# Kernel optimization log

Measured on AMD Instinct MI355X. Metric: run time of the kernel, lower is better.

## Reference

```python
import jax, jax.numpy as jnp
import numpy as np

DIM = 512
HEADS = 16
WIN = (2, 7, 7)
N = WIN[0] * WIN[1] * WIN[2]  # 98
TABLE = (2 * WIN[0] - 1) * (2 * WIN[1] - 1) * (2 * WIN[2] - 1)  # 507


def _rel_pos_index():
    cd, ch, cw = np.arange(WIN[0]), np.arange(WIN[1]), np.arange(WIN[2])
    coords = np.stack(np.meshgrid(cd, ch, cw, indexing='ij'))  # (3, D, H, W)
    flat = coords.reshape(3, -1)  # (3, N)
    rel = flat[:, :, None] - flat[:, None, :]  # (3, N, N)
    rel = rel.transpose(1, 2, 0).copy()
    rel[:, :, 0] += WIN[0] - 1
    rel[:, :, 1] += WIN[1] - 1
    rel[:, :, 2] += WIN[2] - 1
    rel[:, :, 0] *= (2 * WIN[1] - 1) * (2 * WIN[2] - 1)
    rel[:, :, 1] *= 2 * WIN[2] - 1
    return jnp.asarray(rel.sum(-1), dtype=jnp.int32)  # (N, N)


def setup_inputs() -> dict:
    key = jax.random.key(0)
    ks = jax.random.split(key, 7)
    B_ = 1024
    nW = 64
    return {
        'x': jax.random.normal(ks[0], (B_, N, DIM), dtype=jnp.float32),
        'mask': jnp.zeros((nW, N, N), dtype=jnp.float32),
        'qkv_w': jax.random.normal(ks[1], (3 * DIM, DIM), dtype=jnp.float32) * 0.02,
        'qkv_b': jnp.zeros((3 * DIM,), dtype=jnp.float32),
        'proj_w': jax.random.normal(ks[2], (DIM, DIM), dtype=jnp.float32) * 0.02,
        'proj_b': jnp.zeros((DIM,), dtype=jnp.float32),
        'bias_table': jax.random.normal(ks[3], (TABLE, HEADS), dtype=jnp.float32) * 0.02,
        'rel_pos_index': _rel_pos_index(),
    }


def reference(x, mask, qkv_w, qkv_b, proj_w, proj_b, bias_table, rel_pos_index):
    B_, n, C = x.shape
    hd = C // HEADS
    scale = hd ** -0.5
    # qkv projection: (B_, N, 3C) -> (3, B_, H, N, hd)
    qkv = (x @ qkv_w.T + qkv_b).reshape(B_, n, 3, HEADS, hd).transpose(2, 0, 3, 1, 4)
    q, k, v = qkv[0], qkv[1], qkv[2]
    attn = jnp.einsum('bhnd,bhmd->bhnm', q * scale, k)  # (B_, H, N, N)
    # gathered relative position bias: (N, N, H) -> (H, N, N)
    bias = bias_table[rel_pos_index.reshape(-1)].reshape(n, n, HEADS).transpose(2, 0, 1)
    attn = attn + bias[None]
    nW = mask.shape[0]
    attn = attn.reshape(B_ // nW, nW, HEADS, n, n) + mask[None, :, None]
    attn = jax.nn.softmax(attn.reshape(B_, HEADS, n, n), axis=-1)
    out = jnp.einsum('bhnm,bhmd->bnhd', attn, v).reshape(B_, n, C)
    return out @ proj_w.T + proj_b
```

## Files before the change

kernel.cpp:

```cpp
#include <hip/hip_runtime.h>
#include <hip/hip_bf16.h>
#include <stdint.h>

#define DIMC 512
#define NTOK 98

typedef float f32x4 __attribute__((ext_vector_type(4)));
typedef short bf16x8 __attribute__((ext_vector_type(8)));
typedef short bf16x4 __attribute__((ext_vector_type(4)));

__device__ inline unsigned short f2bf(float f) {
    union { float f; uint32_t u; } v; v.f = f;
    uint32_t r = v.u + 0x7fffu + ((v.u >> 16) & 1u);
    return (unsigned short)(r >> 16);
}

__device__ inline bf16x8 cvt8(float4 a, float4 b) {
    bf16x8 r;
    r[0] = (short)f2bf(a.x); r[1] = (short)f2bf(a.y);
    r[2] = (short)f2bf(a.z); r[3] = (short)f2bf(a.w);
    r[4] = (short)f2bf(b.x); r[5] = (short)f2bf(b.y);
    r[6] = (short)f2bf(b.z); r[7] = (short)f2bf(b.w);
    return r;
}

__device__ __forceinline__ void gload16(const void* g, void* l) {
    __builtin_amdgcn_global_load_lds(
        (const __attribute__((address_space(1))) unsigned int*)g,
        (__attribute__((address_space(3))) unsigned int*)l, 16, 0, 0);
}

#define CFENCE() __asm__ __volatile__("" ::: "memory")
#define BARRIER() do { CFENCE(); __builtin_amdgcn_s_barrier(); CFENCE(); } while (0)

__global__ void k_cvt3(const float* __restrict__ s0, unsigned short* __restrict__ d0,
                       const float* __restrict__ s1, unsigned short* __restrict__ d1,
                       const float* __restrict__ s2, unsigned short* __restrict__ d2) {
    int b = blockIdx.x;
    const float* src; unsigned short* dst; int i;
    if (b < 25088)      { src = s0; dst = d0; i = b * 256 + threadIdx.x; }
    else if (b < 25472) { src = s1; dst = d1; i = (b - 25088) * 256 + threadIdx.x; }
    else                { src = s2; dst = d2; i = (b - 25472) * 256 + threadIdx.x; }
    float4 a = *(const float4*)(src + (size_t)i * 8);
    float4 c = *(const float4*)(src + (size_t)i * 8 + 4);
    *(bf16x8*)(dst + (size_t)i * 8) = cvt8(a, c);
}

__global__ void k_bm2(const float* __restrict__ table, const int* __restrict__ idx,
                      const float* __restrict__ mask, float* __restrict__ bm_t) {
    int slice = blockIdx.x;
    int b64 = slice >> 4, h = slice & 15;
    float* dst = bm_t + (size_t)slice * 12544;
    const float* mp = mask + (size_t)b64 * 9604;
    for (int t = threadIdx.x; t < 12544; t += blockDim.x) {
        int i = t / 112, c = t - i * 112;
        float v = -1e9f;
        if (c < NTOK && i < NTOK)
            v = (table[idx[i * NTOK + c] * 16 + h] + mp[i * NTOK + c])
                * 1.4426950408889634f;
        dst[t] = v;
    }
}

__global__ __launch_bounds__(512, 2)
void k_qkv3(const unsigned short* __restrict__ xb, const unsigned short* __restrict__ wb,
            const float* __restrict__ qb, unsigned short* __restrict__ qkvbuf) {
    __shared__ unsigned short As[2][2][128 * 64];
    __shared__ unsigned short Bs[2][2][128 * 64];
    const int tid = threadIdx.x;
    const int wid = tid >> 6, l = tid & 63, g = l >> 4, li = l & 15;
    const int wm = wid >> 2, wn = wid & 3;
    const int id = blockIdx.x;
    const int xcd = id & 7, local = id >> 3;
    const int mt = xcd * 49 + local / 6;
    const int nt = local - (local / 6) * 6;
    const int m0 = mt * 256, n0 = nt * 256;

    const int srow = tid >> 3;
    const int scg  = tid & 7;
    const int sxor = (scg ^ (srow & 7)) * 8;
    const unsigned short* aG[2][2];
    const unsigned short* bG[2][2];
    #pragma unroll
    for (int h = 0; h < 2; ++h) {
        aG[h][0] = xb + (size_t)(m0 + h * 128 + srow) * DIMC + sxor;
        aG[h][1] = xb + (size_t)(m0 + h * 128 + 64 + srow) * DIMC + sxor;
        bG[h][0] = wb + (size_t)(n0 + h * 128 + srow) * DIMC + sxor;
        bG[h][1] = wb + (size_t)(n0 + h * 128 + 64 + srow) * DIMC + sxor;
    }
    const int lb0 = wid * 512;
    const int lb1 = 4096 + wid * 512;

    const int axor0 = ((0 + g) ^ (li & 7)) * 8;
    const int axor1 = ((4 + g) ^ (li & 7)) * 8;
    const int arow = li * 64;
    const int brow = (wn & 1) * 4096 + li * 64;
    const int bh = wn >> 1;

    f32x4 acc[8][4] = {};

    gload16(bG[0][0], &Bs[0][0][lb0]); gload16(bG[1][0], &Bs[0][1][lb0]);
    gload16(bG[0][1], &Bs[0][0][lb1]); gload16(bG[1][1], &Bs[0][1][lb1]);
    gload16(aG[0][0], &As[0][0][lb0]); gload16(aG[1][0], &As[0][1][lb0]);
    gload16(aG[0][1], &As[0][0][lb1]); gload16(aG[1][1], &As[0][1][lb1]);

    #pragma unroll
    for (int kt = 0; kt < 8; ++kt) {
        const int s = kt & 1, p = s ^ 1;
        const int ko = (kt + 1) * 64;
        bf16x8 bfr[4][2];
        #pragma unroll
        for (int q = 0; q < 4; ++q) {
            const int mq0 = 2 * q;
            bf16x8 a00, a01, a10, a11;
            if (q == 1 || q == 3) {
                a00 = *(const bf16x8*)&As[s][wm][arow + mq0 * 1024 + axor0];
                a01 = *(const bf16x8*)&As[s][wm][arow + mq0 * 1024 + axor1];
                a10 = *(const bf16x8*)&As[s][wm][arow + (mq0 + 1) * 1024 + axor0];
                a11 = *(const bf16x8*)&As[s][wm][arow + (mq0 + 1) * 1024 + axor1];
            }
            if (kt < 7) {
                if (q == 0) { gload16(bG[0][0] + ko, &Bs[p][0][lb0]);
                              gload16(bG[1][0] + ko, &Bs[p][1][lb0]); }
                if (q == 1) { gload16(bG[0][1] + ko, &Bs[p][0][lb1]);
                              gload16(bG[1][1] + ko, &Bs[p][1][lb1]); }
                if (q == 2) { gload16(aG[0][0] + ko, &As[p][0][lb0]);
                              gload16(aG[1][0] + ko, &As[p][1][lb0]); }
                if (q == 3) { gload16(aG[0][1] + ko, &As[p][0][lb1]);
                              gload16(aG[1][1] + ko, &As[p][1][lb1]); }
            }
            if (q == 0) {
                if (kt < 7) __asm__ __volatile__("s_waitcnt vmcnt(4)" ::: "memory");
                else        __asm__ __volatile__("s_waitcnt vmcnt(2)" ::: "memory");
            } else if (q == 2) {
                if (kt < 7) __asm__ __volatile__("s_waitcnt vmcnt(6)" ::: "memory");
                else        __asm__ __volatile__("s_waitcnt vmcnt(0)" ::: "memory");
            } else {
                if (kt < 7) __asm__ __volatile__("s_waitcnt vmcnt(6)" ::: "memory");
            }
            BARRIER();
            if (q == 0) {
                #pragma unroll
                for (int nq = 0; nq < 4; ++nq) {
                    bfr[nq][0] = *(const bf16x8*)&Bs[s][bh][brow + nq * 1024 + axor0];
                    bfr[nq][1] = *(const bf16x8*)&Bs[s][bh][brow + nq * 1024 + axor1];
                }
            }
            if (q == 0 || q == 2) {
                a00 = *(const bf16x8*)&As[s][wm][arow + mq0 * 1024 + axor0];
                a01 = *(const bf16x8*)&As[s][wm][arow + mq0 * 1024 + axor1];
                a10 = *(const bf16x8*)&As[s][wm][arow + (mq0 + 1) * 1024 + axor0];
                a11 = *(const bf16x8*)&As[s][wm][arow + (mq0 + 1) * 1024 + axor1];
            }
            __asm__ __volatile__("s_waitcnt lgkmcnt(0)" ::: "memory");
            __builtin_amdgcn_s_setprio(1);
            #pragma unroll
            for (int nq = 0; nq < 4; ++nq) {
                acc[mq0][nq] = __builtin_amdgcn_mfma_f32_16x16x32_bf16(
                    bfr[nq][0], a00, acc[mq0][nq], 0, 0, 0);
                acc[mq0][nq] = __builtin_amdgcn_mfma_f32_16x16x32_bf16(
                    bfr[nq][1], a01, acc[mq0][nq], 0, 0, 0);
                acc[mq0 + 1][nq] = __builtin_amdgcn_mfma_f32_16x16x32_bf16(
                    bfr[nq][0], a10, acc[mq0 + 1][nq], 0, 0, 0);
                acc[mq0 + 1][nq] = __builtin_amdgcn_mfma_f32_16x16x32_bf16(
                    bfr[nq][1], a11, acc[mq0 + 1][nq], 0, 0, 0);
            }
            __builtin_amdgcn_s_setprio(0);
        }
    }

    #pragma unroll
    for (int mq = 0; mq < 8; ++mq) {
        int row = m0 + wm * 128 + mq * 16 + li;
        unsigned bw = (unsigned)row / 98u;
        unsigned nn_ = (unsigned)row - bw * 98u;
        unsigned short* rbase = qkvbuf + (size_t)bw * 150528u + nn_ * 32u;
        #pragma unroll
        for (int nq = 0; nq < 4; ++nq) {
            int col0 = n0 + wn * 64 + nq * 16 + g * 4;
            int which = col0 >> 9;
            int h = (col0 >> 5) & 15;
            int d0 = col0 & 31;
            float4 bv = *(const float4*)(qb + col0);
            float sc = (which == 0)
                ? (0.17677669529663689f * 1.4426950408889634f) : 1.0f;
            bf16x4 pk;
            pk[0] = (short)f2bf((acc[mq][nq][0] + bv.x) * sc);
            pk[1] = (short)f2bf((acc[mq][nq][1] + bv.y) * sc);
            pk[2] = (short)f2bf((acc[mq][nq][2] + bv.z) * sc);
            pk[3] = (short)f2bf((acc[mq][nq][3] + bv.w) * sc);
            *(bf16x4*)(rbase + (size_t)(h * 3 + which) * 3136u + d0) = pk;
        }
    }
}

__global__ __launch_bounds__(512, 2)
void k_proj3(const unsigned short* __restrict__ qkvbuf,
             const unsigned short* __restrict__ wb,
             const float* __restrict__ pb, float* __restrict__ out) {
    __shared__ unsigned short As[2][2][128 * 64];
    __shared__ unsigned short Bs[2][2][128 * 64];
    const int tid = threadIdx.x;
    const int wid = tid >> 6, l = tid & 63, g = l >> 4, li = l & 15;
    const int wm = wid >> 2, wn = wid & 3;
    const int id = blockIdx.x;
    const int xcd = id & 7, local = id >> 3;
    const int mt = xcd * 49 + local / 2;
    const int nt = local & 1;
    const int m0 = mt * 256, n0 = nt * 256;

    const int srow = tid >> 3;
    const int scg  = tid & 7;
    const int cgx  = scg ^ (srow & 7);
    const unsigned short* aG[2][2];
    const unsigned short* bG[2][2];
    #pragma unroll
    for (int h = 0; h < 2; ++h) {
        #pragma unroll
        for (int i = 0; i < 2; ++i) {
            int R = m0 + h * 128 + i * 64 + srow;
            unsigned bw = (unsigned)R / 98u, nn = (unsigned)R - bw * 98u;
            aG[h][i] = qkvbuf + (size_t)bw * 150528u + nn * 32u
                       + (size_t)(cgx >> 2) * 9408u + (cgx & 3) * 8;
            bG[h][i] = wb + (size_t)(n0 + h * 128 + i * 64 + srow) * DIMC + cgx * 8;
        }
    }
    const int lb0 = wid * 512;
    const int lb1 = 4096 + wid * 512;

    const int axor0 = ((0 + g) ^ (li & 7)) * 8;
    const int axor1 = ((4 + g) ^ (li & 7)) * 8;
    const int arow = li * 64;
    const int brow = (wn & 1) * 4096 + li * 64;
    const int bh = wn >> 1;

    f32x4 acc[8][4] = {};

    gload16(bG[0][0], &Bs[0][0][lb0]); gload16(bG[1][0], &Bs[0][1][lb0]);
    gload16(bG[0][1], &Bs[0][0][lb1]); gload16(bG[1][1], &Bs[0][1][lb1]);
    gload16(aG[0][0], &As[0][0][lb0]); gload16(aG[1][0], &As[0][1][lb0]);
    gload16(aG[0][1], &As[0][0][lb1]); gload16(aG[1][1], &As[0][1][lb1]);

    #pragma unroll
    for (int kt = 0; kt < 8; ++kt) {
        const int s = kt & 1, p = s ^ 1;
        const size_t ao = (size_t)(kt + 1) * 18816u;
        const int ko = (kt + 1) * 64;
        bf16x8 bfr[4][2];
        #pragma unroll
        for (int q = 0; q < 4; ++q) {
            const int mq0 = 2 * q;
            bf16x8 a00, a01, a10, a11;
            if (q == 1 || q == 3) {
                a00 = *(const bf16x8*)&As[s][wm][arow + mq0 * 1024 + axor0];
                a01 = *(const bf16x8*)&As[s][wm][arow + mq0 * 1024 + axor1];
                a10 = *(const bf16x8*)&As[s][wm][arow + (mq0 + 1) * 1024 + axor0];
                a11 = *(const bf16x8*)&As[s][wm][arow + (mq0 + 1) * 1024 + axor1];
            }
            if (kt < 7) {
                if (q == 0) { gload16(bG[0][0] + ko, &Bs[p][0][lb0]);
                              gload16(bG[1][0] + ko, &Bs[p][1][lb0]); }
                if (q == 1) { gload16(bG[0][1] + ko, &Bs[p][0][lb1]);
                              gload16(bG[1][1] + ko, &Bs[p][1][lb1]); }
                if (q == 2) { gload16(aG[0][0] + ao, &As[p][0][lb0]);
                              gload16(aG[1][0] + ao, &As[p][1][lb0]); }
                if (q == 3) { gload16(aG[0][1] + ao, &As[p][0][lb1]);
                              gload16(aG[1][1] + ao, &As[p][1][lb1]); }
            }
            if (q == 0) {
                if (kt < 7) __asm__ __volatile__("s_waitcnt vmcnt(4)" ::: "memory");
                else        __asm__ __volatile__("s_waitcnt vmcnt(2)" ::: "memory");
            } else if (q == 2) {
                if (kt < 7) __asm__ __volatile__("s_waitcnt vmcnt(6)" ::: "memory");
                else        __asm__ __volatile__("s_waitcnt vmcnt(0)" ::: "memory");
            } else {
                if (kt < 7) __asm__ __volatile__("s_waitcnt vmcnt(6)" ::: "memory");
            }
            BARRIER();
            if (q == 0) {
                #pragma unroll
                for (int nq = 0; nq < 4; ++nq) {
                    bfr[nq][0] = *(const bf16x8*)&Bs[s][bh][brow + nq * 1024 + axor0];
                    bfr[nq][1] = *(const bf16x8*)&Bs[s][bh][brow + nq * 1024 + axor1];
                }
            }
            if (q == 0 || q == 2) {
                a00 = *(const bf16x8*)&As[s][wm][arow + mq0 * 1024 + axor0];
                a01 = *(const bf16x8*)&As[s][wm][arow + mq0 * 1024 + axor1];
                a10 = *(const bf16x8*)&As[s][wm][arow + (mq0 + 1) * 1024 + axor0];
                a11 = *(const bf16x8*)&As[s][wm][arow + (mq0 + 1) * 1024 + axor1];
            }
            __asm__ __volatile__("s_waitcnt lgkmcnt(0)" ::: "memory");
            __builtin_amdgcn_s_setprio(1);
            #pragma unroll
            for (int nq = 0; nq < 4; ++nq) {
                acc[mq0][nq] = __builtin_amdgcn_mfma_f32_16x16x32_bf16(
                    bfr[nq][0], a00, acc[mq0][nq], 0, 0, 0);
                acc[mq0][nq] = __builtin_amdgcn_mfma_f32_16x16x32_bf16(
                    bfr[nq][1], a01, acc[mq0][nq], 0, 0, 0);
                acc[mq0 + 1][nq] = __builtin_amdgcn_mfma_f32_16x16x32_bf16(
                    bfr[nq][0], a10, acc[mq0 + 1][nq], 0, 0, 0);
                acc[mq0 + 1][nq] = __builtin_amdgcn_mfma_f32_16x16x32_bf16(
                    bfr[nq][1], a11, acc[mq0 + 1][nq], 0, 0, 0);
            }
            __builtin_amdgcn_s_setprio(0);
        }
    }

    #pragma unroll
    for (int mq = 0; mq < 8; ++mq) {
        int row2 = m0 + wm * 128 + mq * 16 + li;
        float* orow = out + (size_t)row2 * DIMC;
        #pragma unroll
        for (int nq = 0; nq < 4; ++nq) {
            int col0 = n0 + wn * 64 + nq * 16 + g * 4;
            float4 bv = *(const float4*)(pb + col0);
            float4 v;
            v.x = acc[mq][nq][0] + bv.x;
            v.y = acc[mq][nq][1] + bv.y;
            v.z = acc[mq][nq][2] + bv.z;
            v.w = acc[mq][nq][3] + bv.w;
            *(float4*)(orow + col0) = v;
        }
    }
}

__global__ __launch_bounds__(448)
void k_attn4(unsigned short* __restrict__ qkvbuf, const float* __restrict__ bm_t) {
    __shared__ short Ks[2][112][36];
    __shared__ short Vt[2][32][132];
    __shared__ short Ps[7][16][132];

    const int tid = threadIdx.x;
    const int w = tid >> 6, l = tid & 63, g = l >> 4, li = l & 15;

    const int id = blockIdx.x;
    const int slice = id >> 1, mh = id & 1;

    const float* bmp = bm_t + (size_t)slice * 12544 + (16 * w + li) * 112 + g * 4;
    f32x4 bmf[7];
    #pragma unroll
    for (int j = 0; j < 7; ++j)
        bmf[j] = *(const f32x4*)(bmp + 16 * j);

    #pragma unroll
    for (int bsel = 0; bsel < 2; ++bsel) {
        Ks[bsel][98 + (tid >> 5)][tid & 31] = 0;
        for (int t2 = tid; t2 < 32 * 34; t2 += 448) {
            int d = t2 / 34, c = t2 % 34;
            Vt[bsel][d][98 + c] = 0;
        }
    }
    {
        bf16x4 z = {};
        *(bf16x4*)&Ps[w][li][112 + g * 4] = z;
    }

    const int krow = tid >> 2, kseg = (tid & 3) * 8;
    const size_t step = (size_t)1024 * 9408;
    unsigned short* qslot = qkvbuf + (size_t)(mh * 8192 + slice) * 9408;

    bf16x8 kreg = {}, vreg = {}, aqc, aqn;
    if (tid < 392) {
        kreg = *(const bf16x8*)(qslot + 3136 + krow * 32 + kseg);
        vreg = *(const bf16x8*)(qslot + 6272 + krow * 32 + kseg);
    }
    aqc = *(const bf16x8*)(qslot + (16 * w + li) * 32 + g * 8);
    if (tid < 392) {
        *(bf16x8*)&Ks[0][krow][kseg] = kreg;
        #pragma unroll
        for (int j = 0; j < 8; ++j) Vt[0][kseg + j][krow] = vreg[j];
    }

    for (int it = 0; it < 8; ++it) {
        const int b = it & 1;
        __syncthreads();

        unsigned short* qnext = qslot + step;
        if (it < 7) {
            if (tid < 392) {
                kreg = *(const bf16x8*)(qnext + 3136 + krow * 32 + kseg);
                vreg = *(const bf16x8*)(qnext + 6272 + krow * 32 + kseg);
            }
            aqn = *(const bf16x8*)(qnext + (16 * w + li) * 32 + g * 8);
        }

        f32x4 s[7];
        __builtin_amdgcn_s_setprio(1);
        #pragma unroll
        for (int j = 0; j < 7; ++j) {
            bf16x8 bk = *(bf16x8*)&Ks[b][16 * j + li][g * 8];
            s[j] = __builtin_amdgcn_mfma_f32_16x16x32_bf16(bk, aqc, bmf[j], 0, 0, 0);
        }
        __builtin_amdgcn_s_setprio(0);

        float p[7][4];
        float sum = 0.f;
        #pragma unroll
        for (int j = 0; j < 7; ++j)
            #pragma unroll
            for (int r = 0; r < 4; ++r) {
                p[j][r] = exp2f(s[j][r]);
                sum += p[j][r];
            }
        sum += __shfl_xor(sum, 16);
        sum += __shfl_xor(sum, 32);
        float sinv = 1.0f / sum;

        #pragma unroll
        for (int j = 0; j < 7; ++j) {
            bf16x4 pk;
            pk[0] = (short)f2bf(p[j][0] * sinv);
            pk[1] = (short)f2bf(p[j][1] * sinv);
            pk[2] = (short)f2bf(p[j][2] * sinv);
            pk[3] = (short)f2bf(p[j][3] * sinv);
            *(bf16x4*)&Ps[w][li][16 * j + g * 4] = pk;
        }

        __asm__ __volatile__("s_waitcnt lgkmcnt(0)" ::: "memory");
        __builtin_amdgcn_sched_barrier(0);

        f32x4 o[2] = {};
        __builtin_amdgcn_s_setprio(1);
        #pragma unroll
        for (int ks = 0; ks < 4; ++ks) {
            bf16x8 pa = *(bf16x8*)&Ps[w][li][ks * 32 + g * 8];
            #pragma unroll
            for (int ct = 0; ct < 2; ++ct) {
                bf16x8 vb = *(bf16x8*)&Vt[b][ct * 16 + li][ks * 32 + g * 8];
                o[ct] = __builtin_amdgcn_mfma_f32_16x16x32_bf16(pa, vb, o[ct], 0, 0, 0);
            }
        }
        __builtin_amdgcn_s_setprio(0);

        #pragma unroll
        for (int ct = 0; ct < 2; ++ct) {
            #pragma unroll
            for (int r = 0; r < 4; ++r) {
                int i = 16 * w + g * 4 + r;
                if (i < NTOK) {
                    int d = ct * 16 + li;
                    qslot[i * 32 + d] = f2bf(o[ct][r]);
                }
            }
        }

        if (it < 7) {
            if (tid < 392) {
                *(bf16x8*)&Ks[b ^ 1][krow][kseg] = kreg;
                #pragma unroll
                for (int j = 0; j < 8; ++j) Vt[b ^ 1][kseg + j][krow] = vreg[j];
            }
            aqc = aqn;
            qslot = qnext;
        }
    }
}

__global__ void k_bias(const float* __restrict__ table, const int* __restrict__ idx,
                       float* __restrict__ bias_full) {
    int h = blockIdx.x, i = blockIdx.y, j = threadIdx.x;
    if (j < NTOK)
        bias_full[(h * NTOK + i) * NTOK + j] = table[idx[i * NTOK + j] * 16 + h];
}

__global__ __launch_bounds__(256)
void k_qkv_old(const float* __restrict__ x, const float* __restrict__ w,
               const float* __restrict__ qb, unsigned short* __restrict__ qkvbuf) {
    __shared__ short As[128][36];
    __shared__ short Bs[128][36];
    const int tid = threadIdx.x;
    const int m0 = blockIdx.x * 128, n0 = blockIdx.y * 128;
    const int wid = tid >> 6, l = tid & 63;
    const int wr = wid >> 1, wc = wid & 1;
    const int g = l >> 4, li = l & 15;
    const int srow = tid >> 1, scol = (tid & 1) * 16;

    f32x4 acc[4][4] = {};
    const float* ap = x + (size_t)(m0 + srow) * DIMC + scol;
    const float* bp = w + (size_t)(n0 + srow) * DIMC + scol;

    for (int k0 = 0; k0 < DIMC; k0 += 32) {
        float4 a0 = *(const float4*)(ap + k0);
        float4 a1 = *(const float4*)(ap + k0 + 4);
        float4 a2 = *(const float4*)(ap + k0 + 8);
        float4 a3 = *(const float4*)(ap + k0 + 12);
        float4 b0 = *(const float4*)(bp + k0);
        float4 b1 = *(const float4*)(bp + k0 + 4);
        float4 b2 = *(const float4*)(bp + k0 + 8);
        float4 b3 = *(const float4*)(bp + k0 + 12);
        *(bf16x8*)&As[srow][scol]     = cvt8(a0, a1);
        *(bf16x8*)&As[srow][scol + 8] = cvt8(a2, a3);
        *(bf16x8*)&Bs[srow][scol]     = cvt8(b0, b1);
        *(bf16x8*)&Bs[srow][scol + 8] = cvt8(b2, b3);
        __syncthreads();
        bf16x8 af[4], bfr[4];
        #pragma unroll
        for (int mm = 0; mm < 4; ++mm)
            af[mm] = *(bf16x8*)&As[wr * 64 + mm * 16 + li][g * 8];
        #pragma unroll
        for (int nn = 0; nn < 4; ++nn)
            bfr[nn] = *(bf16x8*)&Bs[wc * 64 + nn * 16 + li][g * 8];
        #pragma unroll
        for (int mm = 0; mm < 4; ++mm)
            #pragma unroll
            for (int nn = 0; nn < 4; ++nn)
                acc[mm][nn] = __builtin_amdgcn_mfma_f32_16x16x32_bf16(
                    af[mm], bfr[nn], acc[mm][nn], 0, 0, 0);
        __syncthreads();
    }

    #pragma unroll
    for (int mm = 0; mm < 4; ++mm) {
        #pragma unroll
        for (int nn = 0; nn < 4; ++nn) {
            int col = n0 + wc * 64 + nn * 16 + li;
            int which = col >> 9;
            int h = (col >> 5) & 15;
            int d = col & 31;
            float bv = qb[col];
            #pragma unroll
            for (int r = 0; r < 4; ++r) {
                int row = m0 + wr * 64 + mm * 16 + g * 4 + r;
                unsigned bw = (unsigned)row / 98u;
                unsigned nn_ = (unsigned)row - bw * 98u;
                float v = acc[mm][nn][r] + bv;
                if (which == 0) v *= 0.17677669529663689f;
                qkvbuf[(size_t)((bw * 16u + h) * 3u + which) * 3136u + nn_ * 32u + d] =
                    f2bf(v);
            }
        }
    }
}

__global__ __launch_bounds__(448)
void k_attn_old(unsigned short* __restrict__ qkvbuf, const float* __restrict__ mask,
                const float* __restrict__ bias_full) {
    __shared__ short Ks[112][36];
    __shared__ short Vt[32][132];
    __shared__ short Ps[7][16][132];

    const int tid = threadIdx.x;
    const int w = tid >> 6, l = tid & 63, g = l >> 4, li = l & 15;
    const int bh = blockIdx.x;
    const int b = bh >> 4, h = bh & 15;

    unsigned short* qslot = qkvbuf + (size_t)bh * 3 * 3136;
    const unsigned short* kslot = qslot + 3136;
    const unsigned short* vslot = qslot + 6272;

    if (tid < 392) {
        int row = tid >> 2, seg = (tid & 3) * 8;
        bf16x8 kv = *(const bf16x8*)(kslot + row * 32 + seg);
        *(bf16x8*)&Ks[row][seg] = kv;
        bf16x8 vv = *(const bf16x8*)(vslot + row * 32 + seg);
        #pragma unroll
        for (int j = 0; j < 8; ++j) Vt[seg + j][row] = vv[j];
    }
    Ks[98 + (tid >> 5)][tid & 31] = 0;
    for (int t2 = tid; t2 < 32 * 34; t2 += 448) {
        int d = t2 / 34, c = t2 % 34;
        Vt[d][98 + c] = 0;
    }
    for (int t2 = l; t2 < 16 * 20; t2 += 64) {
        int r = t2 / 20, c = t2 % 20;
        Ps[w][r][112 + c] = 0;
    }

    bf16x8 aq = *(const bf16x8*)(qslot + (16 * w + li) * 32 + g * 8);

    __syncthreads();

    f32x4 s[7];
    #pragma unroll
    for (int j = 0; j < 7; ++j) {
        bf16x8 bk = *(bf16x8*)&Ks[16 * j + li][g * 8];
        f32x4 z = {};
        s[j] = __builtin_amdgcn_mfma_f32_16x16x32_bf16(aq, bk, z, 0, 0, 0);
    }

    const float* bp = bias_full + h * 9604;
    const float* mp = mask + (b & 63) * 9604;
    float sinv[4];
    #pragma unroll
    for (int r = 0; r < 4; ++r) {
        int i = 16 * w + g * 4 + r;
        bool rowok = (i < NTOK);
        float sv[7];
        float mx = -1e30f;
        #pragma unroll
        for (int j = 0; j < 7; ++j) {
            int col = 16 * j + li;
            float t = s[j][r];
            if (rowok && col < NTOK) t += bp[i * NTOK + col] + mp[i * NTOK + col];
            else t = -1e30f;
            sv[j] = t;
            mx = fmaxf(mx, t);
        }
        mx = fmaxf(mx, __shfl_xor(mx, 1));
        mx = fmaxf(mx, __shfl_xor(mx, 2));
        mx = fmaxf(mx, __shfl_xor(mx, 4));
        mx = fmaxf(mx, __shfl_xor(mx, 8));
        float sum = 0.f;
        #pragma unroll
        for (int j = 0; j < 7; ++j) {
            float p = __expf(sv[j] - mx);
            sum += p;
            Ps[w][g * 4 + r][16 * j + li] = (short)f2bf(p);
        }
        sum += __shfl_xor(sum, 1);
        sum += __shfl_xor(sum, 2);
        sum += __shfl_xor(sum, 4);
        sum += __shfl_xor(sum, 8);
        sinv[r] = 1.0f / sum;
    }

    __syncthreads();

    f32x4 o[2] = {};
    #pragma unroll
    for (int ks = 0; ks < 4; ++ks) {
        bf16x8 pa = *(bf16x8*)&Ps[w][li][ks * 32 + g * 8];
        #pragma unroll
        for (int ct = 0; ct < 2; ++ct) {
            bf16x8 vb = *(bf16x8*)&Vt[ct * 16 + li][ks * 32 + g * 8];
            o[ct] = __builtin_amdgcn_mfma_f32_16x16x32_bf16(pa, vb, o[ct], 0, 0, 0);
        }
    }

    #pragma unroll
    for (int ct = 0; ct < 2; ++ct) {
        #pragma unroll
        for (int r = 0; r < 4; ++r) {
            int i = 16 * w + g * 4 + r;
            if (i < NTOK) {
                int d = ct * 16 + li;
                qslot[i * 32 + d] = f2bf(o[ct][r] * sinv[r]);
            }
        }
    }
}

__global__ __launch_bounds__(256)
void k_proj_old(const unsigned short* __restrict__ qkvbuf, const float* __restrict__ w,
                const float* __restrict__ pb, float* __restrict__ out) {
    __shared__ short As[128][36];
    __shared__ short Bs[128][36];
    const int tid = threadIdx.x;
    const int m0 = blockIdx.x * 128, n0 = blockIdx.y * 128;
    const int wid = tid >> 6, l = tid & 63;
    const int wr = wid >> 1, wc = wid & 1;
    const int g = l >> 4, li = l & 15;
    const int srow = tid >> 1, scol = (tid & 1) * 16;

    unsigned row = m0 + srow;
    unsigned bw = row / 98u, nn_ = row - bw * 98u;
    const unsigned short* abase =
        qkvbuf + (size_t)bw * 48u * 3136u + (size_t)nn_ * 32u + scol;
    const float* bp = w + (size_t)(n0 + srow) * DIMC + scol;

    f32x4 acc[4][4] = {};

    for (int k0 = 0; k0 < DIMC; k0 += 32) {
        int hh = k0 >> 5;
        const unsigned short* ap = abase + (size_t)hh * 9408u;
        bf16x8 A0 = *(const bf16x8*)ap;
        bf16x8 A1 = *(const bf16x8*)(ap + 8);
        float4 b0 = *(const float4*)(bp + k0);
        float4 b1 = *(const float4*)(bp + k0 + 4);
        float4 b2 = *(const float4*)(bp + k0 + 8);
        float4 b3 = *(const float4*)(bp + k0 + 12);
        *(bf16x8*)&As[srow][scol]     = A0;
        *(bf16x8*)&As[srow][scol + 8] = A1;
        *(bf16x8*)&Bs[srow][scol]     = cvt8(b0, b1);
        *(bf16x8*)&Bs[srow][scol + 8] = cvt8(b2, b3);
        __syncthreads();
        bf16x8 af[4], bfr[4];
        #pragma unroll
        for (int mm = 0; mm < 4; ++mm)
            af[mm] = *(bf16x8*)&As[wr * 64 + mm * 16 + li][g * 8];
        #pragma unroll
        for (int nn = 0; nn < 4; ++nn)
            bfr[nn] = *(bf16x8*)&Bs[wc * 64 + nn * 16 + li][g * 8];
        #pragma unroll
        for (int mm = 0; mm < 4; ++mm)
            #pragma unroll
            for (int nn = 0; nn < 4; ++nn)
                acc[mm][nn] = __builtin_amdgcn_mfma_f32_16x16x32_bf16(
                    af[mm], bfr[nn], acc[mm][nn], 0, 0, 0);
        __syncthreads();
    }

    #pragma unroll
    for (int mm = 0; mm < 4; ++mm) {
        #pragma unroll
        for (int nn = 0; nn < 4; ++nn) {
            int col = n0 + wc * 64 + nn * 16 + li;
            float bv = pb[col];
            #pragma unroll
            for (int r = 0; r < 4; ++r) {
                int row2 = m0 + wr * 64 + mm * 16 + g * 4 + r;
                out[(size_t)row2 * DIMC + col] = acc[mm][nn][r] + bv;
            }
        }
    }
}

extern "C" void kernel_launch(void* const* d_in, const int* in_sizes, int n_in,
                              void* d_out, int out_size, void* d_ws, size_t ws_size,
                              hipStream_t stream) {
    const float* x          = (const float*)d_in[0];
    const float* mask       = (const float*)d_in[1];
    const float* qkv_w      = (const float*)d_in[2];
    const float* qkv_b      = (const float*)d_in[3];
    const float* proj_w     = (const float*)d_in[4];
    const float* proj_b     = (const float*)d_in[5];
    const float* bias_table = (const float*)d_in[6];
    const int*   rel_idx    = (const int*)d_in[7];
    float* out = (float*)d_out;

    const size_t QKV_BYTES = (size_t)16384 * 3 * 3136 * 2;
    const size_t XB_BYTES  = (size_t)100352 * 512 * 2;
    const size_t WQ_BYTES  = (size_t)1536 * 512 * 2;
    const size_t WP_BYTES  = (size_t)512 * 512 * 2;

    unsigned short* qkvbuf = (unsigned short*)d_ws;
    const size_t need = QKV_BYTES + XB_BYTES + WQ_BYTES + WP_BYTES;

    if (ws_size >= need) {
        unsigned short* xb  = (unsigned short*)((char*)d_ws + QKV_BYTES);
        unsigned short* wqb = xb + (size_t)100352 * 512;
        unsigned short* wpb = wqb + (size_t)1536 * 512;
        float* bm_t = (float*)xb;

        k_cvt3<<<dim3(25600), dim3(256), 0, stream>>>(x, xb, qkv_w, wqb, proj_w, wpb);

        k_qkv3<<<dim3(2352), dim3(512), 0, stream>>>(xb, wqb, qkv_b, qkvbuf);
        k_bm2<<<dim3(1024), dim3(256), 0, stream>>>(bias_table, rel_idx, mask, bm_t);
        k_attn4<<<dim3(2048), dim3(448), 0, stream>>>(qkvbuf, bm_t);
        k_proj3<<<dim3(784), dim3(512), 0, stream>>>(qkvbuf, wpb, proj_b, out);
    } else {
        float* bias_full = (float*)((char*)d_ws + QKV_BYTES);
        k_bias<<<dim3(16, 98), dim3(128), 0, stream>>>(bias_table, rel_idx, bias_full);
        k_qkv_old<<<dim3(784, 12), dim3(256), 0, stream>>>(x, qkv_w, qkv_b, qkvbuf);
        k_attn_old<<<dim3(16384), dim3(448), 0, stream>>>(qkvbuf, mask, bias_full);
        k_proj_old<<<dim3(784, 4), dim3(256), 0, stream>>>(qkvbuf, proj_w, proj_b, out);
    }
}
```

Measured before the change: 545.9 us.

## Shrink QKV and proj GEMM tiles to 128x128 with simpler double buffering

Both GEMM kernels move from 256x256 tiles with 8 waves and a finely interleaved per-quarter load schedule to 128x128 tiles with 4 waves. Each k-step now issues the whole next stage up front, then waits and synchronises with two barriers. The grid becomes four times larger, giving more blocks for load balance and occupancy. The cost is lower arithmetic intensity per tile, more global and L2 traffic, and less overlap of loads with MFMA work.

```diff
diff --git a/kernel.cpp b/kernel.cpp
--- a/kernel.cpp
+++ b/kernel.cpp
@@ -62,116 +62,79 @@
     }
 }
 
-__global__ __launch_bounds__(512, 2)
-void k_qkv3(const unsigned short* __restrict__ xb, const unsigned short* __restrict__ wb,
+__global__ __launch_bounds__(256, 2)
+void k_qkv4(const unsigned short* __restrict__ xb, const unsigned short* __restrict__ wb,
             const float* __restrict__ qb, unsigned short* __restrict__ qkvbuf) {
-    __shared__ unsigned short As[2][2][128 * 64];
-    __shared__ unsigned short Bs[2][2][128 * 64];
+    __shared__ unsigned short As[2][128 * 64];
+    __shared__ unsigned short Bs[2][128 * 64];
     const int tid = threadIdx.x;
     const int wid = tid >> 6, l = tid & 63, g = l >> 4, li = l & 15;
-    const int wm = wid >> 2, wn = wid & 3;
+    const int wm = wid >> 1, wn = wid & 1;
     const int id = blockIdx.x;
     const int xcd = id & 7, local = id >> 3;
-    const int mt = xcd * 49 + local / 6;
-    const int nt = local - (local / 6) * 6;
-    const int m0 = mt * 256, n0 = nt * 256;
+    const int mt = xcd * 98 + local / 12;
+    const int nt = local - (local / 12) * 12;
+    const int m0 = mt * 128, n0 = nt * 128;
 
     const int srow = tid >> 3;
     const int scg  = tid & 7;
     const int sxor = (scg ^ (srow & 7)) * 8;
-    const unsigned short* aG[2][2];
-    const unsigned short* bG[2][2];
-    #pragma unroll
-    for (int h = 0; h < 2; ++h) {
-        aG[h][0] = xb + (size_t)(m0 + h * 128 + srow) * DIMC + sxor;
-        aG[h][1] = xb + (size_t)(m0 + h * 128 + 64 + srow) * DIMC + sxor;
-        bG[h][0] = wb + (size_t)(n0 + h * 128 + srow) * DIMC + sxor;
-        bG[h][1] = wb + (size_t)(n0 + h * 128 + 64 + srow) * DIMC + sxor;
-    }
-    const int lb0 = wid * 512;
-    const int lb1 = 4096 + wid * 512;
+    const unsigned short* aGb = xb + (size_t)(m0 + srow) * DIMC + sxor;
+    const unsigned short* bGb = wb + (size_t)(n0 + srow) * DIMC + sxor;
+    const int lds_base = wid * 512;
 
     const int axor0 = ((0 + g) ^ (li & 7)) * 8;
     const int axor1 = ((4 + g) ^ (li & 7)) * 8;
-    const int arow = li * 64;
-    const int brow = (wn & 1) * 4096 + li * 64;
-    const int bh = wn >> 1;
-
-    f32x4 acc[8][4] = {};
-
-    gload16(bG[0][0], &Bs[0][0][lb0]); gload16(bG[1][0], &Bs[0][1][lb0]);
-    gload16(bG[0][1], &Bs[0][0][lb1]); gload16(bG[1][1], &Bs[0][1][lb1]);
-    gload16(aG[0][0], &As[0][0][lb0]); gload16(aG[1][0], &As[0][1][lb0]);
-    gload16(aG[0][1], &As[0][0][lb1]); gload16(aG[1][1], &As[0][1][lb1]);
-
+    const int arow = (wm * 64 + li) * 64;
+    const int brow = (wn * 64 + li) * 64;
+
+    f32x4 acc[4][4] = {};
+
+#define QSTAGE(s, ko) do {                                                   \
+        _Pragma("unroll")                                                    \
+        for (int r = 0; r < 4; ++r) {                                        \
+            gload16(aGb + (size_t)(r * 32) * DIMC + (ko), &As[s][r * 2048 + lds_base]); \
+            gload16(bGb + (size_t)(r * 32) * DIMC + (ko), &Bs[s][r * 2048 + lds_base]); \
+        } } while (0)
+
+    QSTAGE(0, 0);
     #pragma unroll
     for (int kt = 0; kt < 8; ++kt) {
-        const int s = kt & 1, p = s ^ 1;
-        const int ko = (kt + 1) * 64;
+        const int s = kt & 1;
+        if (kt < 7) {
+            QSTAGE(s ^ 1, (kt + 1) * 64);
+            __asm__ __volatile__("s_waitcnt vmcnt(8)" ::: "memory");
+        } else {
+            __asm__ __volatile__("s_waitcnt vmcnt(0)" ::: "memory");
+        }
+        BARRIER();
         bf16x8 bfr[4][2];
         #pragma unroll
-        for (int q = 0; q < 4; ++q) {
-            const int mq0 = 2 * q;
-            bf16x8 a00, a01, a10, a11;
-            if (q == 1 || q == 3) {
-                a00 = *(const bf16x8*)&As[s][wm][arow + mq0 * 1024 + axor0];
-                a01 = *(const bf16x8*)&As[s][wm][arow + mq0 * 1024 + axor1];
-                a10 = *(const bf16x8*)&As[s][wm][arow + (mq0 + 1) * 1024 + axor0];
-                a11 = *(const bf16x8*)&As[s][wm][arow + (mq0 + 1) * 1024 + axor1];
-            }
-            if (kt < 7) {
-                if (q == 0) { gload16(bG[0][0] + ko, &Bs[p][0][lb0]);
-                              gload16(bG[1][0] + ko, &Bs[p][1][lb0]); }
-                if (q == 1) { gload16(bG[0][1] + ko, &Bs[p][0][lb1]);
-                              gload16(bG[1][1] + ko, &Bs[p][1][lb1]); }
-                if (q == 2) { gload16(aG[0][0] + ko, &As[p][0][lb0]);
-                              gload16(aG[1][0] + ko, &As[p][1][lb0]); }
-                if (q == 3) { gload16(aG[0][1] + ko, &As[p][0][lb1]);
-                              gload16(aG[1][1] + ko, &As[p][1][lb1]); }
-            }
-            if (q == 0) {
-                if (kt < 7) __asm__ __volatile__("s_waitcnt vmcnt(4)" ::: "memory");
-                else        __asm__ __volatile__("s_waitcnt vmcnt(2)" ::: "memory");
-            } else if (q == 2) {
-                if (kt < 7) __asm__ __volatile__("s_waitcnt vmcnt(6)" ::: "memory");
-                else        __asm__ __volatile__("s_waitcnt vmcnt(0)" ::: "memory");
-            } else {
-                if (kt < 7) __asm__ __volatile__("s_waitcnt vmcnt(6)" ::: "memory");
-            }
-            BARRIER();
-            if (q == 0) {
-                #pragma unroll
-                for (int nq = 0; nq < 4; ++nq) {
-                    bfr[nq][0] = *(const bf16x8*)&Bs[s][bh][brow + nq * 1024 + axor0];
-                    bfr[nq][1] = *(const bf16x8*)&Bs[s][bh][brow + nq * 1024 + axor1];
-                }
-            }
-            if (q == 0 || q == 2) {
-                a00 = *(const bf16x8*)&As[s][wm][arow + mq0 * 1024 + axor0];
-                a01 = *(const bf16x8*)&As[s][wm][arow + mq0 * 1024 + axor1];
-                a10 = *(const bf16x8*)&As[s][wm][arow + (mq0 + 1) * 1024 + axor0];
-                a11 = *(const bf16x8*)&As[s][wm][arow + (mq0 + 1) * 1024 + axor1];
-            }
-            __asm__ __volatile__("s_waitcnt lgkmcnt(0)" ::: "memory");
+        for (int nq = 0; nq < 4; ++nq) {
+            bfr[nq][0] = *(const bf16x8*)&Bs[s][brow + nq * 1024 + axor0];
+            bfr[nq][1] = *(const bf16x8*)&Bs[s][brow + nq * 1024 + axor1];
+        }
+        #pragma unroll
+        for (int mq = 0; mq < 4; ++mq) {
+            bf16x8 a0 = *(const bf16x8*)&As[s][arow + mq * 1024 + axor0];
+            bf16x8 a1 = *(const bf16x8*)&As[s][arow + mq * 1024 + axor1];
             __builtin_amdgcn_s_setprio(1);
             #pragma unroll
             for (int nq = 0; nq < 4; ++nq) {
-                acc[mq0][nq] = __builtin_amdgcn_mfma_f32_16x16x32_bf16(
-                    bfr[nq][0], a00, acc[mq0][nq], 0, 0, 0);
-                acc[mq0][nq] = __builtin_amdgcn_mfma_f32_16x16x32_bf16(
-                    bfr[nq][1], a01, acc[mq0][nq], 0, 0, 0);
-                acc[mq0 + 1][nq] = __builtin_amdgcn_mfma_f32_16x16x32_bf16(
-                    bfr[nq][0], a10, acc[mq0 + 1][nq], 0, 0, 0);
-                acc[mq0 + 1][nq] = __builtin_amdgcn_mfma_f32_16x16x32_bf16(
-                    bfr[nq][1], a11, acc[mq0 + 1][nq], 0, 0, 0);
+                acc[mq][nq] = __builtin_amdgcn_mfma_f32_16x16x32_bf16(
+                    bfr[nq][0], a0, acc[mq][nq], 0, 0, 0);
+                acc[mq][nq] = __builtin_amdgcn_mfma_f32_16x16x32_bf16(
+                    bfr[nq][1], a1, acc[mq][nq], 0, 0, 0);
             }
             __builtin_amdgcn_s_setprio(0);
         }
-    }
-
-    #pragma unroll
-    for (int mq = 0; mq < 8; ++mq) {
-        int row = m0 + wm * 128 + mq * 16 + li;
+        BARRIER();
+    }
+#undef QSTAGE
+
+    #pragma unroll
+    for (int mq = 0; mq < 4; ++mq) {
+        int row = m0 + wm * 64 + mq * 16 + li;
         unsigned bw = (unsigned)row / 98u;
         unsigned nn_ = (unsigned)row - bw * 98u;
         unsigned short* rbase = qkvbuf + (size_t)bw * 150528u + nn_ * 32u;
@@ -194,122 +157,88 @@
     }
 }
 
-__global__ __launch_bounds__(512, 2)
-void k_proj3(const unsigned short* __restrict__ qkvbuf,
+__global__ __launch_bounds__(256, 2)
+void k_proj4(const unsigned short* __restrict__ qkvbuf,
              const unsigned short* __restrict__ wb,
              const float* __restrict__ pb, float* __restrict__ out) {
-    __shared__ unsigned short As[2][2][128 * 64];
-    __shared__ unsigned short Bs[2][2][128 * 64];
+    __shared__ unsigned short As[2][128 * 64];
+    __shared__ unsigned short Bs[2][128 * 64];
     const int tid = threadIdx.x;
     const int wid = tid >> 6, l = tid & 63, g = l >> 4, li = l & 15;
-    const int wm = wid >> 2, wn = wid & 3;
+    const int wm = wid >> 1, wn = wid & 1;
     const int id = blockIdx.x;
     const int xcd = id & 7, local = id >> 3;
-    const int mt = xcd * 49 + local / 2;
-    const int nt = local & 1;
-    const int m0 = mt * 256, n0 = nt * 256;
+    const int mt = xcd * 98 + local / 4;
+    const int nt = local & 3;
+    const int m0 = mt * 128, n0 = nt * 128;
 
     const int srow = tid >> 3;
     const int scg  = tid & 7;
     const int cgx  = scg ^ (srow & 7);
-    const unsigned short* aG[2][2];
-    const unsigned short* bG[2][2];
-    #pragma unroll
-    for (int h = 0; h < 2; ++h) {
-        #pragma unroll
-        for (int i = 0; i < 2; ++i) {
-            int R = m0 + h * 128 + i * 64 + srow;
-            unsigned bw = (unsigned)R / 98u, nn = (unsigned)R - bw * 98u;
-            aG[h][i] = qkvbuf + (size_t)bw * 150528u + nn * 32u
-                       + (size_t)(cgx >> 2) * 9408u + (cgx & 3) * 8;
-            bG[h][i] = wb + (size_t)(n0 + h * 128 + i * 64 + srow) * DIMC + cgx * 8;
-        }
-    }
-    const int lb0 = wid * 512;
-    const int lb1 = 4096 + wid * 512;
+    const unsigned short* aG[4];
+    const unsigned short* bG[4];
+    #pragma unroll
+    for (int r = 0; r < 4; ++r) {
+        int R = m0 + r * 32 + srow;
+        unsigned bw = (unsigned)R / 98u, nn = (unsigned)R - bw * 98u;
+        aG[r] = qkvbuf + (size_t)bw * 150528u + nn * 32u
+                + (size_t)(cgx >> 2) * 9408u + (cgx & 3) * 8;
+        bG[r] = wb + (size_t)(n0 + r * 32 + srow) * DIMC + cgx * 8;
+    }
+    const int lds_base = wid * 512;
 
     const int axor0 = ((0 + g) ^ (li & 7)) * 8;
     const int axor1 = ((4 + g) ^ (li & 7)) * 8;
-    const int arow = li * 64;
-    const int brow = (wn & 1) * 4096 + li * 64;
-    const int bh = wn >> 1;
-
-    f32x4 acc[8][4] = {};
-
-    gload16(bG[0][0], &Bs[0][0][lb0]); gload16(bG[1][0], &Bs[0][1][lb0]);
-    gload16(bG[0][1], &Bs[0][0][lb1]); gload16(bG[1][1], &Bs[0][1][lb1]);
-    gload16(aG[0][0], &As[0][0][lb0]); gload16(aG[1][0], &As[0][1][lb0]);
-    gload16(aG[0][1], &As[0][0][lb1]); gload16(aG[1][1], &As[0][1][lb1]);
-
+    const int arow = (wm * 64 + li) * 64;
+    const int brow = (wn * 64 + li) * 64;
+
+    f32x4 acc[4][4] = {};
+
+#define PSTAGE(s, kt) do {                                                   \
+        _Pragma("unroll")                                                    \
+        for (int r = 0; r < 4; ++r) {                                        \
+            gload16(aG[r] + (size_t)(kt) * 18816u, &As[s][r * 2048 + lds_base]); \
+            gload16(bG[r] + (kt) * 64, &Bs[s][r * 2048 + lds_base]);         \
+        } } while (0)
+
+    PSTAGE(0, 0);
     #pragma unroll
     for (int kt = 0; kt < 8; ++kt) {
-        const int s = kt & 1, p = s ^ 1;
-        const size_t ao = (size_t)(kt + 1) * 18816u;
-        const int ko = (kt + 1) * 64;
+        const int s = kt & 1;
+        if (kt < 7) {
+            PSTAGE(s ^ 1, kt + 1);
+            __asm__ __volatile__("s_waitcnt vmcnt(8)" ::: "memory");
+        } else {
+            __asm__ __volatile__("s_waitcnt vmcnt(0)" ::: "memory");
+        }
+        BARRIER();
         bf16x8 bfr[4][2];
         #pragma unroll
-        for (int q = 0; q < 4; ++q) {
-            const int mq0 = 2 * q;
-            bf16x8 a00, a01, a10, a11;
-            if (q == 1 || q == 3) {
-                a00 = *(const bf16x8*)&As[s][wm][arow + mq0 * 1024 + axor0];
-                a01 = *(const bf16x8*)&As[s][wm][arow + mq0 * 1024 + axor1];
-                a10 = *(const bf16x8*)&As[s][wm][arow + (mq0 + 1) * 1024 + axor0];
-                a11 = *(const bf16x8*)&As[s][wm][arow + (mq0 + 1) * 1024 + axor1];
-            }
-            if (kt < 7) {
-                if (q == 0) { gload16(bG[0][0] + ko, &Bs[p][0][lb0]);
-                              gload16(bG[1][0] + ko, &Bs[p][1][lb0]); }
-                if (q == 1) { gload16(bG[0][1] + ko, &Bs[p][0][lb1]);
-                              gload16(bG[1][1] + ko, &Bs[p][1][lb1]); }
-                if (q == 2) { gload16(aG[0][0] + ao, &As[p][0][lb0]);
-                              gload16(aG[1][0] + ao, &As[p][1][lb0]); }
-                if (q == 3) { gload16(aG[0][1] + ao, &As[p][0][lb1]);
-                              gload16(aG[1][1] + ao, &As[p][1][lb1]); }
-            }
-            if (q == 0) {
-                if (kt < 7) __asm__ __volatile__("s_waitcnt vmcnt(4)" ::: "memory");
-                else        __asm__ __volatile__("s_waitcnt vmcnt(2)" ::: "memory");
-            } else if (q == 2) {
-                if (kt < 7) __asm__ __volatile__("s_waitcnt vmcnt(6)" ::: "memory");
-                else        __asm__ __volatile__("s_waitcnt vmcnt(0)" ::: "memory");
-            } else {
-                if (kt < 7) __asm__ __volatile__("s_waitcnt vmcnt(6)" ::: "memory");
-            }
-            BARRIER();
-            if (q == 0) {
-                #pragma unroll
-                for (int nq = 0; nq < 4; ++nq) {
-                    bfr[nq][0] = *(const bf16x8*)&Bs[s][bh][brow + nq * 1024 + axor0];
-                    bfr[nq][1] = *(const bf16x8*)&Bs[s][bh][brow + nq * 1024 + axor1];
-                }
-            }
-            if (q == 0 || q == 2) {
-                a00 = *(const bf16x8*)&As[s][wm][arow + mq0 * 1024 + axor0];
-                a01 = *(const bf16x8*)&As[s][wm][arow + mq0 * 1024 + axor1];
-                a10 = *(const bf16x8*)&As[s][wm][arow + (mq0 + 1) * 1024 + axor0];
-                a11 = *(const bf16x8*)&As[s][wm][arow + (mq0 + 1) * 1024 + axor1];
-            }
-            __asm__ __volatile__("s_waitcnt lgkmcnt(0)" ::: "memory");
+        for (int nq = 0; nq < 4; ++nq) {
+            bfr[nq][0] = *(const bf16x8*)&Bs[s][brow + nq * 1024 + axor0];
+            bfr[nq][1] = *(const bf16x8*)&Bs[s][brow + nq * 1024 + axor1];
+        }
+        #pragma unroll
+        for (int mq = 0; mq < 4; ++mq) {
+            bf16x8 a0 = *(const bf16x8*)&As[s][arow + mq * 1024 + axor0];
+            bf16x8 a1 = *(const bf16x8*)&As[s][arow + mq * 1024 + axor1];
             __builtin_amdgcn_s_setprio(1);
             #pragma unroll
             for (int nq = 0; nq < 4; ++nq) {
-                acc[mq0][nq] = __builtin_amdgcn_mfma_f32_16x16x32_bf16(
-                    bfr[nq][0], a00, acc[mq0][nq], 0, 0, 0);
-                acc[mq0][nq] = __builtin_amdgcn_mfma_f32_16x16x32_bf16(
-                    bfr[nq][1], a01, acc[mq0][nq], 0, 0, 0);
-                acc[mq0 + 1][nq] = __builtin_amdgcn_mfma_f32_16x16x32_bf16(
-                    bfr[nq][0], a10, acc[mq0 + 1][nq], 0, 0, 0);
-                acc[mq0 + 1][nq] = __builtin_amdgcn_mfma_f32_16x16x32_bf16(
-                    bfr[nq][1], a11, acc[mq0 + 1][nq], 0, 0, 0);
+                acc[mq][nq] = __builtin_amdgcn_mfma_f32_16x16x32_bf16(
+                    bfr[nq][0], a0, acc[mq][nq], 0, 0, 0);
+                acc[mq][nq] = __builtin_amdgcn_mfma_f32_16x16x32_bf16(
+                    bfr[nq][1], a1, acc[mq][nq], 0, 0, 0);
             }
             __builtin_amdgcn_s_setprio(0);
         }
-    }
-
-    #pragma unroll
-    for (int mq = 0; mq < 8; ++mq) {
-        int row2 = m0 + wm * 128 + mq * 16 + li;
+        BARRIER();
+    }
+#undef PSTAGE
+
+    #pragma unroll
+    for (int mq = 0; mq < 4; ++mq) {
+        int row2 = m0 + wm * 64 + mq * 16 + li;
         float* orow = out + (size_t)row2 * DIMC;
         #pragma unroll
         for (int nq = 0; nq < 4; ++nq) {
@@ -735,10 +664,10 @@
 
         k_cvt3<<<dim3(25600), dim3(256), 0, stream>>>(x, xb, qkv_w, wqb, proj_w, wpb);
 
-        k_qkv3<<<dim3(2352), dim3(512), 0, stream>>>(xb, wqb, qkv_b, qkvbuf);
+        k_qkv4<<<dim3(9408), dim3(256), 0, stream>>>(xb, wqb, qkv_b, qkvbuf);
         k_bm2<<<dim3(1024), dim3(256), 0, stream>>>(bias_table, rel_idx, mask, bm_t);
         k_attn4<<<dim3(2048), dim3(448), 0, stream>>>(qkvbuf, bm_t);
-        k_proj3<<<dim3(784), dim3(512), 0, stream>>>(qkvbuf, wpb, proj_b, out);
+        k_proj4<<<dim3(3136), dim3(256), 0, stream>>>(qkvbuf, wpb, proj_b, out);
     } else {
         float* bias_full = (float*)((char*)d_ws + QKV_BYTES);
         k_bias<<<dim3(16, 98), dim3(128), 0, stream>>>(bias_table, rel_idx, bias_full);
```

Result: slower. 591.0 us (+8.3%).
